# Performance work log

Measured on AMD Instinct MI355X. Metric: run time of the kernel, lower is better.

The kernel has to match this reference:

```python
import jax, jax.numpy as jnp
import numpy as np

B, T, D = 2, 2048, 2048
N, K, H = 8, 4, 256
WINDOW = 1024
BASE_FREQ = 10000
ROPE_PROP = 1.0
SCALE_FACTOR = 1.0
K_MASK = -2.3819763e+38


def apply_rope(inputs, positions, base_frequency, scale_factor=1.0, rope_proportion=1.0):
    # inputs: [B,L,N,H], positions: [B,L]
    head_dim = inputs.shape[-1]
    rope_angles = int(rope_proportion * head_dim // 2)
    nope_angles = head_dim // 2 - rope_angles
    freq_exponents = 2.0 / head_dim * jnp.arange(rope_angles, dtype=jnp.float32)
    timescale = jnp.pad(base_frequency ** freq_exponents, (0, nope_angles),
                        mode='constant', constant_values=(0, jnp.inf))
    sinusoid = positions[..., None].astype(jnp.float32) / timescale[None, None, :]
    sinusoid = sinusoid[..., None, :] / scale_factor  # [B,L,1,H//2]
    sin = jnp.sin(sinusoid)
    cos = jnp.cos(sinusoid)
    first, second = jnp.split(inputs, 2, axis=-1)
    out = jnp.concatenate([first * cos - second * sin,
                           second * cos + first * sin], axis=-1)
    return out.astype(inputs.dtype)


def rms_norm(x, scale, eps=1e-6):
    var = jnp.mean(jnp.square(x.astype(jnp.float32)), axis=-1, keepdims=True)
    normed = x * jax.lax.rsqrt(var + eps)
    return (normed * (1.0 + scale)).astype(x.dtype)


def setup_inputs() -> dict:
    key = jax.random.key(0)
    ks = jax.random.split(key, 5)
    std = 0.02
    return {
        'x': jax.random.normal(ks[0], (B, T, D), jnp.float32),
        'positions': jnp.broadcast_to(jnp.arange(T, dtype=jnp.int32), (B, T)),
        'q_w': jax.random.normal(ks[1], (N, D, H), jnp.float32) * std,
        'k_w': jax.random.normal(ks[2], (K, D, H), jnp.float32) * std,
        'v_w': jax.random.normal(ks[3], (K, D, H), jnp.float32) * std,
        'o_w': jax.random.normal(ks[4], (N, H, D), jnp.float32) * std,
        'q_norm_scale': jnp.zeros((H,), jnp.float32),
        'k_norm_scale': jnp.zeros((H,), jnp.float32),
    }


def reference(x, positions, q_w, k_w, v_w, o_w, q_norm_scale, k_norm_scale):
    # QKV projections (Einsum modules)
    q = jnp.einsum('btd,ndh->btnh', x, q_w)   # [B,T,N,H]
    k = jnp.einsum('bsd,kdh->bskh', x, k_w)   # [B,S,K,H]
    v = jnp.einsum('bsd,kdh->bskh', x, v_w)
    # QK RMSNorm (gemma-style, zero-centered scale)
    q = rms_norm(q, q_norm_scale)
    k = rms_norm(k, k_norm_scale)
    # RoPE (local attention: base 10000, full proportion)
    q = apply_rope(q, positions, BASE_FREQ, SCALE_FACTOR, ROPE_PROP)
    k = apply_rope(k, positions, BASE_FREQ, SCALE_FACTOR, ROPE_PROP)
    q = q * (H ** -0.5)
    # GQA: group queries over kv heads
    G = N // K
    qg = q.reshape(B, T, K, G, H)
    logits = jnp.einsum('btkgh,bskh->btkgs', qg, k)  # [B,T,K,G,S]
    # causal + sliding-window mask from positions
    qp = positions[:, :, None]
    kp = positions[:, None, :]
    mask = (kp <= qp) & (kp > qp - WINDOW)           # [B,T,S]
    logits = jnp.where(mask[:, :, None, None, :], logits, K_MASK)
    probs = jax.nn.softmax(logits.astype(jnp.float32), axis=-1).astype(logits.dtype)
    out = jnp.einsum('btkgs,bskh->btkgh', probs, v).reshape(B, T, N, H)
    return jnp.einsum('btnh,nhd->btd', out, o_w)
```

## Files before the change

### kernel.cpp

```cpp
#include <hip/hip_runtime.h>
#include <cmath>

#define T_SEQ 2048
#define WINDOW 1024

typedef __attribute__((ext_vector_type(8))) short bf16x8;
typedef __attribute__((ext_vector_type(4))) float f32x4;
typedef __attribute__((ext_vector_type(16))) float f32x16;

__device__ __forceinline__ unsigned short f2bf(float f) {
  union { float f; unsigned int u; } v; v.f = f;
  unsigned int r = v.u + 0x7FFFu + ((v.u >> 16) & 1u);
  return (unsigned short)(r >> 16);
}
__device__ __forceinline__ float bf2f(unsigned short u) {
  union { unsigned int i; float f; } v; v.i = ((unsigned int)u) << 16;
  return v.f;
}

#define GLD16(gp, lp)                                                  \
  __builtin_amdgcn_global_load_lds(                                    \
      (__attribute__((address_space(1))) unsigned int*)(gp),           \
      (__attribute__((address_space(3))) unsigned int*)(lp), 16, 0, 0)

__global__ __launch_bounds__(256) void prep(
    const float* __restrict__ x,
    const float* __restrict__ qw, const float* __restrict__ kw,
    const float* __restrict__ vw, const float* __restrict__ ow,
    unsigned short* __restrict__ xb, unsigned short* __restrict__ wqkvt,
    unsigned short* __restrict__ wot) {
  __shared__ float tile[64][65];
  const int blk = blockIdx.x;
  const int tid = threadIdx.x;
  if (blk < 8192) {
    size_t i = (size_t)blk * 256 + tid;
    float4 v = *(const float4*)&x[i * 4];
    ushort4 o;
    o.x = f2bf(v.x); o.y = f2bf(v.y); o.z = f2bf(v.z); o.w = f2bf(v.w);
    *(ushort4*)&xb[i * 4] = o;
    return;
  }
  int tx = tid & 15, ty = tid >> 4;
  if (blk < 10240) {
    int idx = blk - 8192;
    int c0 = (idx & 63) * 64, d0 = (idx >> 6) * 64;
    const float* src; int hbase;
    if (c0 < 2048) { src = qw + (size_t)(c0 >> 8) * 524288; hbase = c0 & 255; }
    else if (c0 < 3072) { int cc = c0 - 2048; src = kw + (size_t)(cc >> 8) * 524288; hbase = cc & 255; }
    else { int cc = c0 - 3072; src = vw + (size_t)(cc >> 8) * 524288; hbase = cc & 255; }
#pragma unroll
    for (int p = 0; p < 4; ++p) {
      float4 v = *(const float4*)&src[(size_t)(d0 + ty + 16 * p) * 256 + hbase + tx * 4];
      tile[ty + 16 * p][tx * 4 + 0] = v.x; tile[ty + 16 * p][tx * 4 + 1] = v.y;
      tile[ty + 16 * p][tx * 4 + 2] = v.z; tile[ty + 16 * p][tx * 4 + 3] = v.w;
    }
    __syncthreads();
#pragma unroll
    for (int p = 0; p < 4; ++p) {
      int hh = ty + 16 * p;
      ushort4 o;
      o.x = f2bf(tile[tx * 4 + 0][hh]); o.y = f2bf(tile[tx * 4 + 1][hh]);
      o.z = f2bf(tile[tx * 4 + 2][hh]); o.w = f2bf(tile[tx * 4 + 3][hh]);
      *(ushort4*)&wqkvt[(size_t)(c0 + hh) * 2048 + d0 + tx * 4] = o;
    }
  } else {
    int idx = blk - 10240;
    int j0 = (idx & 31) * 64, d0 = (idx >> 5) * 64;
#pragma unroll
    for (int p = 0; p < 4; ++p) {
      float4 v = *(const float4*)&ow[(size_t)(j0 + ty + 16 * p) * 2048 + d0 + tx * 4];
      tile[ty + 16 * p][tx * 4 + 0] = v.x; tile[ty + 16 * p][tx * 4 + 1] = v.y;
      tile[ty + 16 * p][tx * 4 + 2] = v.z; tile[ty + 16 * p][tx * 4 + 3] = v.w;
    }
    __syncthreads();
#pragma unroll
    for (int p = 0; p < 4; ++p) {
      int hh = ty + 16 * p;
      ushort4 o;
      o.x = f2bf(tile[tx * 4 + 0][hh]); o.y = f2bf(tile[tx * 4 + 1][hh]);
      o.z = f2bf(tile[tx * 4 + 2][hh]); o.w = f2bf(tile[tx * 4 + 3][hh]);
      *(ushort4*)&wot[(size_t)(d0 + hh) * 2048 + j0 + tx * 4] = o;
    }
  }
}

__device__ __forceinline__ void gemm128_core(
    const unsigned short* __restrict__ A, const unsigned short* __restrict__ Bt,
    unsigned short* As, unsigned short* Bs, int m0, int n0, int K,
    f32x4 acc[4][4]) {
  const int tid = threadIdx.x;
  const int wave = tid >> 6, lane = tid & 63;
  const int wm = (wave & 1) << 6, wn = (wave >> 1) << 6;
  const int i0 = wave * 2, i1 = wave * 2 + 1;
  const int sr = lane >> 2;
  const int sc = (lane & 3) * 8;
  const size_t ar0 = (size_t)(m0 + i0 * 16 + sr) * K + sc;
  const size_t ar1 = (size_t)(m0 + i1 * 16 + sr) * K + sc;
  const size_t br0 = (size_t)(n0 + i0 * 16 + sr) * K + sc;
  const size_t br1 = (size_t)(n0 + i1 * 16 + sr) * K + sc;
  const int fm = lane & 15, fk = (lane >> 4) * 8;

  for (int kt = 0; kt < K; kt += 32) {
    GLD16(A + ar0 + kt, As + i0 * 512);
    GLD16(A + ar1 + kt, As + i1 * 512);
    GLD16(Bt + br0 + kt, Bs + i0 * 512);
    GLD16(Bt + br1 + kt, Bs + i1 * 512);
    __syncthreads();
    bf16x8 af[4], bv[4];
#pragma unroll
    for (int i = 0; i < 4; ++i)
      af[i] = *(const bf16x8*)&As[(wm + i * 16 + fm) * 32 + fk];
#pragma unroll
    for (int j = 0; j < 4; ++j)
      bv[j] = *(const bf16x8*)&Bs[(wn + j * 16 + fm) * 32 + fk];
#pragma unroll
    for (int i = 0; i < 4; ++i)
#pragma unroll
      for (int j = 0; j < 4; ++j)
        acc[i][j] = __builtin_amdgcn_mfma_f32_16x16x32_bf16(af[i], bv[j], acc[i][j], 0, 0, 0);
    __syncthreads();
  }
}

__global__ __launch_bounds__(256) void gemm_qkv_bf16(
    const unsigned short* __restrict__ xb, const unsigned short* __restrict__ wt,
    unsigned short* __restrict__ qo, unsigned short* __restrict__ ko,
    unsigned short* __restrict__ vo) {
  __shared__ unsigned short As[128 * 32];
  __shared__ unsigned short Bs[128 * 32];
  const int n0 = blockIdx.x * 128, m0 = blockIdx.y * 128;
  f32x4 acc[4][4];
#pragma unroll
  for (int i = 0; i < 4; ++i)
#pragma unroll
    for (int j = 0; j < 4; ++j) acc[i][j] = {0.f, 0.f, 0.f, 0.f};
  gemm128_core(xb, wt, As, Bs, m0, n0, 2048, acc);

  unsigned short* obase; int ldo, cb;
  if (n0 < 2048) { obase = qo; ldo = 2048; cb = n0; }
  else if (n0 < 3072) { obase = ko; ldo = 1024; cb = n0 - 2048; }
  else { obase = vo; ldo = 1024; cb = n0 - 3072; }
  const int lane = threadIdx.x & 63, wave = threadIdx.x >> 6;
  const int wm = (wave & 1) << 6, wn = (wave >> 1) << 6;
  const int rbase = m0 + wm + (lane >> 4) * 4;
  const int cbase = cb + wn + (lane & 15);
#pragma unroll
  for (int i = 0; i < 4; ++i)
#pragma unroll
    for (int j = 0; j < 4; ++j)
#pragma unroll
      for (int r = 0; r < 4; ++r)
        obase[(size_t)(rbase + i * 16 + r) * ldo + cbase + j * 16] = f2bf(acc[i][j][r]);
}

__global__ __launch_bounds__(256) void gemm_out_bf16(
    const unsigned short* __restrict__ ab, const unsigned short* __restrict__ wot,
    float* __restrict__ out) {
  __shared__ unsigned short As[128 * 32];
  __shared__ unsigned short Bs[128 * 32];
  const int n0 = blockIdx.x * 128, m0 = blockIdx.y * 128;
  f32x4 acc[4][4];
#pragma unroll
  for (int i = 0; i < 4; ++i)
#pragma unroll
    for (int j = 0; j < 4; ++j) acc[i][j] = {0.f, 0.f, 0.f, 0.f};
  gemm128_core(ab, wot, As, Bs, m0, n0, 2048, acc);

  const int lane = threadIdx.x & 63, wave = threadIdx.x >> 6;
  const int wm = (wave & 1) << 6, wn = (wave >> 1) << 6;
  const int rbase = m0 + wm + (lane >> 4) * 4;
  const int cbase = n0 + wn + (lane & 15);
#pragma unroll
  for (int i = 0; i < 4; ++i)
#pragma unroll
    for (int j = 0; j < 4; ++j)
#pragma unroll
      for (int r = 0; r < 4; ++r)
        out[(size_t)(rbase + i * 16 + r) * 2048 + cbase + j * 16] = acc[i][j][r];
}

__global__ __launch_bounds__(256) void postproc(
    unsigned short* __restrict__ qb, const unsigned short* __restrict__ kb,
    unsigned short* __restrict__ kpan,
    const unsigned short* __restrict__ vbf, unsigned short* __restrict__ vpan,
    const int* __restrict__ positions,
    const float* __restrict__ qns, const float* __restrict__ kns) {
  const int blk = blockIdx.x;
  const int tid = threadIdx.x;
  if (blk < 12288) {
    int row = blk * 4 + (tid >> 6);
    int lane = tid & 63;
    const unsigned short* src; const float* ns; float extra; int bt;
    bool isq = row < 32768;
    if (isq) {
      src = qb + (size_t)row * 256; ns = qns; extra = 0.0625f; bt = row >> 3;
    } else {
      int r = row - 32768;
      src = kb + (size_t)r * 256; ns = kns; extra = 1.0f; bt = r >> 2;
    }
    int pos = positions[bt];

    ushort4 u = *(const ushort4*)&src[lane << 2];
    float xv[4] = {bf2f(u.x), bf2f(u.y), bf2f(u.z), bf2f(u.w)};
    float ss = xv[0]*xv[0] + xv[1]*xv[1] + xv[2]*xv[2] + xv[3]*xv[3];
#pragma unroll
    for (int off = 1; off < 64; off <<= 1) ss += __shfl_xor(ss, off, 64);
    float rinv = rsqrtf(ss * (1.0f / 256.0f) + 1e-6f);

    float4 sc4 = *(const float4*)&ns[lane << 2];
    xv[0] *= rinv * (1.0f + sc4.x);
    xv[1] *= rinv * (1.0f + sc4.y);
    xv[2] *= rinv * (1.0f + sc4.z);
    xv[3] *= rinv * (1.0f + sc4.w);

    float ov[4];
#pragma unroll
    for (int c = 0; c < 4; ++c) ov[c] = __shfl_xor(xv[c], 32, 64);

    int hr = (lane & 31) << 2;
    float sgn = (lane < 32) ? -1.0f : 1.0f;
    ushort4 w4;
    unsigned short res[4];
#pragma unroll
    for (int c = 0; c < 4; ++c) {
      float invts = exp2f(-(float)(hr + c) * 0.10381025296523007f);
      float angle = (float)pos * invts;
      float sn, cs;
      __sincosf(angle, &sn, &cs);
      res[c] = f2bf((xv[c] * cs + sgn * ov[c] * sn) * extra);
    }
    w4.x = res[0]; w4.y = res[1]; w4.z = res[2]; w4.w = res[3];
    if (isq) {
      *(ushort4*)&qb[(size_t)row * 256 + (lane << 2)] = w4;
    } else {
      int r = row - 32768;
      int kvh = r & 3;
      int b_ = bt >> 11, t = bt & 2047;
      unsigned short* pan = kpan + (((size_t)(b_ * 4 + kvh) * 64 + (t >> 5)) * 8192);
      int s = t & 31;
      int c = lane >> 1;
      size_t el = (size_t)s * 256 + (size_t)((c ^ s) & 31) * 8 + (lane & 1) * 4;
      *(ushort4*)&pan[el] = w4;
    }
    return;
  }
  __shared__ unsigned short tile[64][68];
  int idx = blk - 12288;
  int h0 = (idx & 3) * 64;
  int t0 = ((idx >> 2) & 31) * 64;
  int z = idx >> 7;
  int tx = tid & 15, ty = tid >> 4;
  const unsigned short* src = vbf + ((size_t)(z >> 2) * 8192 + (z & 3)) * 256;
#pragma unroll
  for (int p = 0; p < 4; ++p) {
    ushort4 v = *(const ushort4*)&src[(size_t)(t0 + ty + 16 * p) * 1024 + h0 + tx * 4];
    tile[ty + 16 * p][tx * 4 + 0] = v.x; tile[ty + 16 * p][tx * 4 + 1] = v.y;
    tile[ty + 16 * p][tx * 4 + 2] = v.z; tile[ty + 16 * p][tx * 4 + 3] = v.w;
  }
  __syncthreads();
#pragma unroll
  for (int p = 0; p < 4; ++p) {
    int hh = ty + 16 * p;
    int h = h0 + hh;
    int t = t0 + tx * 4;
    int pp = t >> 5, s = t & 31;
    ushort4 o;
    o.x = tile[tx * 4 + 0][hh]; o.y = tile[tx * 4 + 1][hh];
    o.z = tile[tx * 4 + 2][hh]; o.w = tile[tx * 4 + 3][hh];
    size_t el = ((size_t)z * 64 + pp) * 8192 + (size_t)h * 32 +
                (size_t)(((s >> 3) ^ (h & 3)) & 3) * 8 + (s & 7);
    *(ushort4*)&vpan[el] = o;
  }
}

__global__ __launch_bounds__(128) void attn_mfma(
    const unsigned short* __restrict__ qb,
    const unsigned short* __restrict__ kpan,
    const unsigned short* __restrict__ vpan,
    unsigned short* __restrict__ ob) {
  __shared__ __align__(16) unsigned short Kl[8192];
  __shared__ __align__(16) unsigned short Vl[8192];
  __shared__ __align__(16) unsigned short Ps[3072];

  const int tid = threadIdx.x;
  const int w = tid >> 6, lane = tid & 63;
  const int l5 = lane >> 5, l31 = lane & 31;
  const int pair = blockIdx.x & 7;
  const int t0 = (blockIdx.x >> 3) * 32;
  const int kvh = pair >> 1, b = pair & 1;
  const int n = 2 * kvh + w;
  const int tmin = t0, tmax = t0 + 31;

  bf16x8 aq[16];
  {
    const unsigned short* qrow =
        qb + (((size_t)b * 2048 + tmin + l31) * 8 + n) * 256 + l5 * 8;
#pragma unroll
    for (int kc = 0; kc < 16; ++kc) aq[kc] = *(const bf16x8*)(qrow + kc * 16);
  }

  f32x16 O[8], lsum;
#pragma unroll
  for (int i = 0; i < 8; ++i)
#pragma unroll
    for (int r = 0; r < 16; ++r) O[i][r] = 0.f;
#pragma unroll
  for (int r = 0; r < 16; ++r) lsum[r] = 0.f;

  bf16x8 ones;
#pragma unroll
  for (int i = 0; i < 8; ++i) ones[i] = (short)0x3F80;

  const unsigned short* kpb = kpan + (size_t)(b * 4 + kvh) * 64 * 8192;
  const unsigned short* vpb = vpan + (size_t)(b * 4 + kvh) * 64 * 8192;

  int s_lo = t0 - 1024; if (s_lo < 0) s_lo = 0;
  const int s_end = t0 + 32;

  for (int s0 = s_lo; s0 < s_end; s0 += 32) {
    __syncthreads();
    const unsigned short* kp = kpb + (size_t)(s0 >> 5) * 8192;
    const unsigned short* vp = vpb + (size_t)(s0 >> 5) * 8192;
#pragma unroll
    for (int j = 0; j < 8; ++j) {
      int g = j * 128 + tid;
      GLD16(kp + g * 8, Kl + g * 8);
    }
#pragma unroll
    for (int j = 0; j < 8; ++j) {
      int g = j * 128 + tid;
      GLD16(vp + g * 8, Vl + g * 8);
    }
    __syncthreads();

    f32x16 pa, pb;
#pragma unroll
    for (int r = 0; r < 16; ++r) { pa[r] = 0.f; pb[r] = 0.f; }
#pragma unroll
    for (int kc = 0; kc < 16; kc += 2) {
      bf16x8 b0 = *(const bf16x8*)&Kl[l31 * 256 + (((kc * 2 + l5) ^ l31) & 31) * 8];
      bf16x8 b1 = *(const bf16x8*)&Kl[l31 * 256 + ((((kc + 1) * 2 + l5) ^ l31) & 31) * 8];
      pa = __builtin_amdgcn_mfma_f32_32x32x16_bf16(aq[kc], b0, pa, 0, 0, 0);
      pb = __builtin_amdgcn_mfma_f32_32x32x16_bf16(aq[kc + 1], b1, pb, 0, 0, 0);
    }

    bool allvalid = (s0 + 31 <= tmin) && (s0 >= tmax - 1023);
    int scol = s0 + l31;
#pragma unroll
    for (int r = 0; r < 16; ++r) {
      float sv = pa[r] + pb[r];
      float p = exp2f(sv * 1.442695040888963f);
      int m = (r & 3) + 8 * (r >> 2) + 4 * l5;
      if (!allvalid) {
        int dt = (tmin + m) - scol;
        p = (dt >= 0 && dt < 1024) ? p : 0.f;
      }
      Ps[w * 1536 + (l31 >> 4) * 768 + m * 24 + (l31 & 15)] = f2bf(p);
    }

    bf16x8 pf0 = *(const bf16x8*)&Ps[w * 1536 + l31 * 24 + l5 * 8];
    bf16x8 pf1 = *(const bf16x8*)&Ps[w * 1536 + 768 + l31 * 24 + l5 * 8];
    lsum = __builtin_amdgcn_mfma_f32_32x32x16_bf16(pf0, ones, lsum, 0, 0, 0);
    lsum = __builtin_amdgcn_mfma_f32_32x32x16_bf16(pf1, ones, lsum, 0, 0, 0);
#pragma unroll
    for (int hb = 0; hb < 8; ++hb) {
      int row = hb * 32 + l31;
      bf16x8 v0 = *(const bf16x8*)&Vl[row * 32 + ((l5 ^ row) & 3) * 8];
      bf16x8 v1 = *(const bf16x8*)&Vl[row * 32 + (((2 + l5) ^ row) & 3) * 8];
      O[hb] = __builtin_amdgcn_mfma_f32_32x32x16_bf16(pf0, v0, O[hb], 0, 0, 0);
      O[hb] = __builtin_amdgcn_mfma_f32_32x32x16_bf16(pf1, v1, O[hb], 0, 0, 0);
    }
  }

  unsigned short* obase = ob + (((size_t)b * 2048 + tmin) * 8 + n) * 256;
#pragma unroll
  for (int r = 0; r < 16; ++r) {
    int m = (r & 3) + 8 * (r >> 2) + 4 * l5;
    float rinv = 1.0f / lsum[r];
    size_t rowoff = (size_t)m * 2048;
#pragma unroll
    for (int hb = 0; hb < 8; ++hb)
      obase[rowoff + hb * 32 + l31] = f2bf(O[hb][r] * rinv);
  }
}

extern "C" void kernel_launch(void* const* d_in, const int* in_sizes, int n_in,
                              void* d_out, int out_size, void* d_ws, size_t ws_size,
                              hipStream_t stream) {
  const float* x   = (const float*)d_in[0];
  const int* pos   = (const int*)d_in[1];
  const float* q_w = (const float*)d_in[2];
  const float* k_w = (const float*)d_in[3];
  const float* v_w = (const float*)d_in[4];
  const float* o_w = (const float*)d_in[5];
  const float* qns = (const float*)d_in[6];
  const float* kns = (const float*)d_in[7];
  float* out = (float*)d_out;

  unsigned short* W = (unsigned short*)d_ws;
  unsigned short* qb0   = W;
  unsigned short* kb0   = W + 8388608;
  unsigned short* vbf   = W + 12582912;
  unsigned short* vpan  = W + 16777216;
  unsigned short* kpan  = W + 20971520;
  unsigned short* xb    = W + 25165824;
  unsigned short* wqkvt = W + 33554432;
  unsigned short* abuf  = wqkvt;
  unsigned short* wot   = W + 41943040;

  prep<<<dim3(11264), 256, 0, stream>>>(x, q_w, k_w, v_w, o_w, xb, wqkvt, wot);
  gemm_qkv_bf16<<<dim3(32, 32), 256, 0, stream>>>(xb, wqkvt, qb0, kb0, vbf);
  postproc<<<dim3(13312), 256, 0, stream>>>(qb0, kb0, kpan, vbf, vpan, pos, qns, kns);
  attn_mfma<<<dim3(512), 128, 0, stream>>>(qb0, kpan, vpan, abuf);
  gemm_out_bf16<<<dim3(16, 32), 256, 0, stream>>>(abuf, wot, out);
}
```

Measured before the change: 364.9 us.

## Replace QKV GEMM with 256x256-tile, 8-wave pipelined LDS kernel

Swaps the 128x128 single-buffered QKV projection GEMM for a 256x256 tile kernel using 512 threads. It prefetches K-slices into a double-buffered, XOR-swizzled LDS region through direct global-to-LDS loads, and interleaves those loads with MFMA phases using explicit waitcnt, barriers and setprio. A block-index swizzle improves L2 reuse. The aim is to hide load latency, cut LDS bank conflicts and raise arithmetic intensity, at the cost of 128KB of LDS per block (one block per CU) and a single-wave grid of 256 blocks.

```diff
diff --git a/kernel.cpp b/kernel.cpp
--- a/kernel.cpp
+++ b/kernel.cpp
@@ -84,6 +84,145 @@
   }
 }
 
+__global__ __launch_bounds__(512) void gemm_qkv_256(
+    const unsigned short* __restrict__ xb, const unsigned short* __restrict__ wt,
+    unsigned short* __restrict__ qo, unsigned short* __restrict__ ko,
+    unsigned short* __restrict__ vo) {
+  __shared__ unsigned short lds[65536];
+  const int tid = threadIdx.x;
+  const int wave = tid >> 6, lane = tid & 63;
+  const int wr = wave >> 2, wc = wave & 3;
+  const int fm = lane & 15, fk = lane >> 4;
+
+  const int bid = blockIdx.x;
+  const int swz = (bid & 7) * 32 + (bid >> 3);
+  const int m0 = (swz >> 4) * 256, n0 = (swz & 15) * 256;
+
+  const int soff = fm * 32 + ((fk ^ ((fm >> 2) & 3)) << 3);
+  const int aoff = wr * 4096 + soff;
+  const int boff = wc * 2048 + soff;
+
+  const unsigned short* Ab = xb + (size_t)m0 * 2048;
+  const unsigned short* Bb = wt + (size_t)n0 * 2048;
+
+  const int l0 = tid, l1 = tid + 512;
+  const int r0 = l0 >> 2, o0 = l0 & 3;
+  const int r1 = l1 >> 2, o1 = l1 & 3;
+  const int sA0 = r0 * 2048 + ((o0 ^ ((r0 >> 2) & 3)) << 3);
+  const int sA1 = r1 * 2048 + ((o1 ^ ((r1 >> 2) & 3)) << 3);
+
+#define STAGE(srcbase, kofs, dstbase)                  \
+  do {                                                 \
+    GLD16((srcbase) + sA0 + (kofs), (dstbase) + l0 * 8); \
+    GLD16((srcbase) + sA1 + (kofs), (dstbase) + l1 * 8); \
+  } while (0)
+
+  f32x4 acc[8][4];
+#pragma unroll
+  for (int i = 0; i < 8; ++i)
+#pragma unroll
+    for (int j = 0; j < 4; ++j) acc[i][j] = {0.f, 0.f, 0.f, 0.f};
+
+  STAGE(Ab, 0,  lds + 0);
+  STAGE(Bb, 0,  lds + 16384);
+  STAGE(Ab, 32, lds + 8192);
+  STAGE(Bb, 32, lds + 24576);
+  STAGE(Ab, 64, lds + 32768);
+  STAGE(Bb, 64, lds + 49152);
+  asm volatile("s_waitcnt vmcnt(8)" ::: "memory");
+  __builtin_amdgcn_s_barrier();
+
+  for (int t = 0; t < 32; ++t) {
+    const int p = t & 1;
+    unsigned short* base = lds + p * 32768;
+    unsigned short* xbase = lds + (p ^ 1) * 32768;
+    const int t1 = (t < 31) ? t + 1 : 31;
+    const int t2 = (t < 30) ? t + 2 : 31;
+
+    bf16x8 a[4], b[4];
+#pragma unroll
+    for (int i = 0; i < 4; ++i) a[i] = *(const bf16x8*)(base + aoff + i * 512);
+#pragma unroll
+    for (int j = 0; j < 4; ++j) b[j] = *(const bf16x8*)(base + 16384 + boff + j * 512);
+    STAGE(Ab, t1 * 64 + 32, xbase + 8192);
+    __builtin_amdgcn_s_barrier();
+    asm volatile("s_waitcnt lgkmcnt(0)" ::: "memory");
+    __builtin_amdgcn_sched_barrier(0);
+    __builtin_amdgcn_s_setprio(1);
+#pragma unroll
+    for (int i = 0; i < 4; ++i)
+#pragma unroll
+      for (int j = 0; j < 4; ++j)
+        acc[i][j] = __builtin_amdgcn_mfma_f32_16x16x32_bf16(a[i], b[j], acc[i][j], 0, 0, 0);
+    __builtin_amdgcn_s_setprio(0);
+    __builtin_amdgcn_s_barrier();
+
+#pragma unroll
+    for (int i = 0; i < 4; ++i) a[i] = *(const bf16x8*)(base + aoff + (i + 4) * 512);
+    STAGE(Bb, t1 * 64 + 32, xbase + 24576);
+    __builtin_amdgcn_s_barrier();
+    asm volatile("s_waitcnt lgkmcnt(0)" ::: "memory");
+    __builtin_amdgcn_sched_barrier(0);
+    __builtin_amdgcn_s_setprio(1);
+#pragma unroll
+    for (int i = 0; i < 4; ++i)
+#pragma unroll
+      for (int j = 0; j < 4; ++j)
+        acc[i + 4][j] = __builtin_amdgcn_mfma_f32_16x16x32_bf16(a[i], b[j], acc[i + 4][j], 0, 0, 0);
+    __builtin_amdgcn_s_setprio(0);
+    asm volatile("s_waitcnt vmcnt(8)" ::: "memory");
+    __builtin_amdgcn_s_barrier();
+
+#pragma unroll
+    for (int i = 0; i < 4; ++i) a[i] = *(const bf16x8*)(base + 8192 + aoff + i * 512);
+#pragma unroll
+    for (int j = 0; j < 4; ++j) b[j] = *(const bf16x8*)(base + 24576 + boff + j * 512);
+    STAGE(Ab, t2 * 64, base + 0);
+    __builtin_amdgcn_s_barrier();
+    asm volatile("s_waitcnt lgkmcnt(0)" ::: "memory");
+    __builtin_amdgcn_sched_barrier(0);
+    __builtin_amdgcn_s_setprio(1);
+#pragma unroll
+    for (int i = 0; i < 4; ++i)
+#pragma unroll
+      for (int j = 0; j < 4; ++j)
+        acc[i][j] = __builtin_amdgcn_mfma_f32_16x16x32_bf16(a[i], b[j], acc[i][j], 0, 0, 0);
+    __builtin_amdgcn_s_setprio(0);
+    __builtin_amdgcn_s_barrier();
+
+#pragma unroll
+    for (int i = 0; i < 4; ++i) a[i] = *(const bf16x8*)(base + 8192 + aoff + (i + 4) * 512);
+    STAGE(Bb, t2 * 64, base + 16384);
+    __builtin_amdgcn_s_barrier();
+    asm volatile("s_waitcnt lgkmcnt(0)" ::: "memory");
+    __builtin_amdgcn_sched_barrier(0);
+    __builtin_amdgcn_s_setprio(1);
+#pragma unroll
+    for (int i = 0; i < 4; ++i)
+#pragma unroll
+      for (int j = 0; j < 4; ++j)
+        acc[i + 4][j] = __builtin_amdgcn_mfma_f32_16x16x32_bf16(a[i], b[j], acc[i + 4][j], 0, 0, 0);
+    __builtin_amdgcn_s_setprio(0);
+    asm volatile("s_waitcnt vmcnt(8)" ::: "memory");
+    __builtin_amdgcn_s_barrier();
+  }
+#undef STAGE
+
+  unsigned short* obase; int ldo, cb;
+  if (n0 < 2048) { obase = qo; ldo = 2048; cb = n0; }
+  else if (n0 < 3072) { obase = ko; ldo = 1024; cb = n0 - 2048; }
+  else { obase = vo; ldo = 1024; cb = n0 - 3072; }
+  const int rbase = m0 + wr * 128 + (lane >> 4) * 4;
+  const int cbase = cb + wc * 64 + fm;
+#pragma unroll
+  for (int i = 0; i < 8; ++i)
+#pragma unroll
+    for (int j = 0; j < 4; ++j)
+#pragma unroll
+      for (int r = 0; r < 4; ++r)
+        obase[(size_t)(rbase + i * 16 + r) * ldo + cbase + j * 16] = f2bf(acc[i][j][r]);
+}
+
 __device__ __forceinline__ void gemm128_core(
     const unsigned short* __restrict__ A, const unsigned short* __restrict__ Bt,
     unsigned short* As, unsigned short* Bs, int m0, int n0, int K,
@@ -120,37 +259,6 @@
         acc[i][j] = __builtin_amdgcn_mfma_f32_16x16x32_bf16(af[i], bv[j], acc[i][j], 0, 0, 0);
     __syncthreads();
   }
-}
-
-__global__ __launch_bounds__(256) void gemm_qkv_bf16(
-    const unsigned short* __restrict__ xb, const unsigned short* __restrict__ wt,
-    unsigned short* __restrict__ qo, unsigned short* __restrict__ ko,
-    unsigned short* __restrict__ vo) {
-  __shared__ unsigned short As[128 * 32];
-  __shared__ unsigned short Bs[128 * 32];
-  const int n0 = blockIdx.x * 128, m0 = blockIdx.y * 128;
-  f32x4 acc[4][4];
-#pragma unroll
-  for (int i = 0; i < 4; ++i)
-#pragma unroll
-    for (int j = 0; j < 4; ++j) acc[i][j] = {0.f, 0.f, 0.f, 0.f};
-  gemm128_core(xb, wt, As, Bs, m0, n0, 2048, acc);
-
-  unsigned short* obase; int ldo, cb;
-  if (n0 < 2048) { obase = qo; ldo = 2048; cb = n0; }
-  else if (n0 < 3072) { obase = ko; ldo = 1024; cb = n0 - 2048; }
-  else { obase = vo; ldo = 1024; cb = n0 - 3072; }
-  const int lane = threadIdx.x & 63, wave = threadIdx.x >> 6;
-  const int wm = (wave & 1) << 6, wn = (wave >> 1) << 6;
-  const int rbase = m0 + wm + (lane >> 4) * 4;
-  const int cbase = cb + wn + (lane & 15);
-#pragma unroll
-  for (int i = 0; i < 4; ++i)
-#pragma unroll
-    for (int j = 0; j < 4; ++j)
-#pragma unroll
-      for (int r = 0; r < 4; ++r)
-        obase[(size_t)(rbase + i * 16 + r) * ldo + cbase + j * 16] = f2bf(acc[i][j][r]);
 }
 
 __global__ __launch_bounds__(256) void gemm_out_bf16(
@@ -409,7 +517,7 @@
   unsigned short* wot   = W + 41943040;
 
   prep<<<dim3(11264), 256, 0, stream>>>(x, q_w, k_w, v_w, o_w, xb, wqkvt, wot);
-  gemm_qkv_bf16<<<dim3(32, 32), 256, 0, stream>>>(xb, wqkvt, qb0, kb0, vbf);
+  gemm_qkv_256<<<dim3(256), 512, 0, stream>>>(xb, wqkvt, qb0, kb0, vbf);
   postproc<<<dim3(13312), 256, 0, stream>>>(qb0, kb0, kpan, vbf, vpan, pos, qns, kns);
   attn_mfma<<<dim3(512), 128, 0, stream>>>(qb0, kpan, vpan, abuf);
   gemm_out_bf16<<<dim3(16, 32), 256, 0, stream>>>(abuf, wot, out);
```

Measured after the change: 345.4 us. -5.3%, faster.
